# Kernel optimization log

Hardware: AMD Instinct MI355X
Metric: run time of the kernel (lower is better)

The kernel has to match this reference:

```python
import jax, jax.numpy as jnp
import numpy as np

N_NODES = 100000
EPS = 1e-12  # F.normalize eps


def _sage_conv(x, src, dst, deg, Wl, bl, Wr):
    # mean aggregation of neighbor (source) features at destination nodes
    agg = jax.ops.segment_sum(x[src], dst, num_segments=N_NODES)  # [N, F]
    agg = agg / jnp.maximum(deg, 1.0)[:, None]
    out = agg @ Wl + bl + x @ Wr  # lin_l(mean(x_j)) + lin_r(x_i)
    # normalize=True -> L2 row normalization
    norm = jnp.sqrt(jnp.sum(out * out, axis=-1, keepdims=True))
    return out / jnp.maximum(norm, EPS)


def setup_inputs() -> dict:
    key = jax.random.key(0)
    ks = jax.random.split(key, 10)
    F_IN, H, C = 14, 32, 2
    x = jax.random.normal(ks[0], (N_NODES, F_IN), dtype=jnp.float32)
    edge_index = jax.random.randint(ks[1], (2, 6400000), 0, N_NODES, dtype=jnp.int32)
    def glorot(k, shape):
        lim = float(np.sqrt(6.0 / (shape[0] + shape[1])))
        return jax.random.uniform(k, shape, jnp.float32, -lim, lim)
    return {
        "x": x,
        "edge_index": edge_index,
        "W1l": glorot(ks[2], (F_IN, H)), "b1": jnp.zeros((H,), jnp.float32),
        "W1r": glorot(ks[3], (F_IN, H)),
        "W2l": glorot(ks[4], (H, H)), "b2": jnp.zeros((H,), jnp.float32),
        "W2r": glorot(ks[5], (H, H)),
        "Wlin": glorot(ks[6], (H, C)), "blin": jnp.zeros((C,), jnp.float32),
    }


def reference(x, edge_index, W1l, b1, W1r, W2l, b2, W2r, Wlin, blin):
    src, dst = edge_index[0], edge_index[1]
    deg = jax.ops.segment_sum(jnp.ones_like(dst, dtype=x.dtype), dst,
                              num_segments=N_NODES)  # in-degree per node
    h = jax.nn.relu(_sage_conv(x, src, dst, deg, W1l, b1, W1r))
    # dropout p=0.2 is identity at inference
    h = jax.nn.relu(_sage_conv(h, src, dst, deg, W2l, b2, W2r))
    return h @ Wlin + blin  # [N, num_classes]
```

## Files before the change

### kernel.cpp

```cpp
#include <hip/hip_runtime.h>
#include <hip/hip_bf16.h>


#define CHA 16384
#define MAXB 512
#define CAPB 18432

static __device__ __forceinline__ unsigned short f2bf(float f) {
    unsigned u = __float_as_uint(f);
    unsigned r = (u + 0x7FFFu + ((u >> 16) & 1u)) >> 16;
    return (unsigned short)r;
}
#define BF_LO(u) __uint_as_float((u) << 16)
#define BF_HI(u) __uint_as_float((u) & 0xFFFF0000u)

__global__ void cvt_x_bf16(const float* __restrict__ x, unsigned short* __restrict__ xb,
                           int* __restrict__ bcursor, int N, int NB) {
    int idx = blockIdx.x * blockDim.x + threadIdx.x;
    if (idx < NB) bcursor[idx] = idx * CAPB;
    if (idx >= N * 16) return;
    int n = idx >> 4, f = idx & 15;
    float v = (f < 14) ? x[n * 14 + f] : 0.f;
    xb[idx] = f2bf(v);
}

__global__ __launch_bounds__(1024) void partitionA(
        const int* __restrict__ src, const int* __restrict__ dst,
        int* __restrict__ bcursor, unsigned* __restrict__ part, int E, int NB) {
    __shared__ unsigned pk[CHA];
    __shared__ int h[MAXB], lofs[MAXB], cur[MAXB], delta[MAXB], tmp[MAXB];
    int t = threadIdx.x;
    int base = blockIdx.x * CHA;
    int end = base + CHA; if (end > E) end = E;
    int cnt = end - base;

    int ed[16], es[16];
    for (int i = t; i < NB; i += 1024) h[i] = 0;
    __syncthreads();
    #pragma unroll
    for (int i = 0; i < 4; ++i) {
        int j = i * 4096 + t * 4;
        if (j + 4 <= cnt) {
            int4 d4 = *(const int4*)(dst + base + j);
            int4 s4 = *(const int4*)(src + base + j);
            ed[i*4+0] = d4.x; ed[i*4+1] = d4.y; ed[i*4+2] = d4.z; ed[i*4+3] = d4.w;
            es[i*4+0] = s4.x; es[i*4+1] = s4.y; es[i*4+2] = s4.z; es[i*4+3] = s4.w;
            atomicAdd(&h[d4.x >> 8], 1);
            atomicAdd(&h[d4.y >> 8], 1);
            atomicAdd(&h[d4.z >> 8], 1);
            atomicAdd(&h[d4.w >> 8], 1);
        } else {
            #pragma unroll
            for (int k = 0; k < 4; ++k) {
                if (j + k < cnt) {
                    ed[i*4+k] = dst[base + j + k];
                    es[i*4+k] = src[base + j + k];
                    atomicAdd(&h[ed[i*4+k] >> 8], 1);
                } else ed[i*4+k] = -1;
            }
        }
    }
    __syncthreads();
    int v = 0;
    if (t < MAXB) { v = (t < NB) ? h[t] : 0; tmp[t] = v; }
    __syncthreads();
    for (int off = 1; off < MAXB; off <<= 1) {
        int a = 0;
        if (t < MAXB && t >= off) a = tmp[t - off];
        __syncthreads();
        if (t < MAXB) tmp[t] += a;
        __syncthreads();
    }
    if (t < NB) {
        int excl = tmp[t] - v;
        lofs[t] = excl;
        cur[t] = excl;
        int g = v ? atomicAdd(&bcursor[t], v) : 0;
        delta[t] = g - excl;
    }
    __syncthreads();
    #pragma unroll
    for (int i = 0; i < 16; ++i) {
        int d = ed[i];
        if (d >= 0) {
            int b = d >> 8;
            int r = atomicAdd(&cur[b], 1);
            pk[r] = ((unsigned)(d & 255) << 24) | (unsigned)es[i];
        }
    }
    __syncthreads();
    int wid = t >> 6, lane = t & 63;
    for (int b = wid; b < NB; b += 16) {
        int s = lofs[b];
        int e2 = (b + 1 < NB) ? lofs[b + 1] : cnt;
        int dlt = delta[b];
        int lim = (b + 1) * CAPB;
        for (int k = s + lane; k < e2; k += 64) {
            int gidx = dlt + k;
            if (gidx < lim) part[gidx] = pk[k];
        }
    }
}

__global__ __launch_bounds__(1024) void partitionB_fused(
        const unsigned* __restrict__ part, const int* __restrict__ bcursor,
        const uint4* __restrict__ xb4, const float* __restrict__ x,
        const float* __restrict__ W1l, const float* __restrict__ b1,
        const float* __restrict__ W1r,
        int* __restrict__ deg, int* __restrict__ offs, int* __restrict__ nlo,
        int* __restrict__ sorted_src, float* __restrict__ hbuf,
        unsigned short* __restrict__ hb, int N, int HALF) {
    __shared__ int pk2[CAPB];
    __shared__ int hh[512], tmp[512], keyofs[512];
    __shared__ int lstart[256], ldeg[256];
    __shared__ float sagg[256 * 17];
    __shared__ float sx[256 * 14];
    __shared__ float swl[448], swr[448], sb1[32];
    int b = blockIdx.x;
    int t = threadIdx.x;
    int start = b * CAPB;
    int end = bcursor[b];
    if (end > start + CAPB) end = start + CAPB;
    int cnt = end - start;
    unsigned ce[18];
    if (t < 512) hh[t] = 0;
    if (t < 448) { swl[t] = W1l[t]; swr[t] = W1r[t]; }
    else if (t < 480) sb1[t - 448] = b1[t - 448];
    __syncthreads();
    #pragma unroll
    for (int i = 0; i < 18; ++i) {
        int idx = start + t + i * 1024;
        unsigned p = 0xFFFFFFFFu;
        if (idx < end) {
            p = part[idx];
            int key = (int)(p >> 24) * 2 + (((int)(p & 0xFFFFFFu) < HALF) ? 0 : 1);
            atomicAdd(&hh[key], 1);
        }
        ce[i] = p;
    }
    {
        int nnod = N - b * 256; if (nnod > 256) nnod = 256; if (nnod < 0) nnod = 0;
        const float* gx = x + (size_t)b * 256 * 14;
        for (int i = t; i < nnod * 14; i += 1024) sx[i] = gx[i];
    }
    __syncthreads();
    int v = (t < 512) ? hh[t] : 0;
    if (t < 512) tmp[t] = v;
    __syncthreads();
    for (int off = 1; off < 512; off <<= 1) {
        int a2 = (t < 512 && t >= off) ? tmp[t - off] : 0;
        __syncthreads();
        if (t < 512) tmp[t] += a2;
        __syncthreads();
    }
    if (t < 512) keyofs[t] = tmp[t] - v;
    __syncthreads();
    if (t < 256) {
        int lo = hh[2 * t];
        int d = lo + hh[2 * t + 1];
        int excl = keyofs[2 * t];
        lstart[t] = excl;
        ldeg[t] = d;
        int node = b * 256 + t;
        if (node < N) {
            deg[node] = d;
            offs[node] = start + excl;
            nlo[node] = lo;
        }
    }
    __syncthreads();
    #pragma unroll
    for (int i = 0; i < 18; ++i) {
        unsigned p = ce[i];
        if (p != 0xFFFFFFFFu) {
            int s = (int)(p & 0xFFFFFFu);
            int key = (int)(p >> 24) * 2 + ((s < HALF) ? 0 : 1);
            int r = atomicAdd(&keyofs[key], 1);
            pk2[r] = s;
        }
    }
    __syncthreads();
    for (int i = t; i < cnt; i += 1024)
        sorted_src[start + i] = pk2[i];

    int node = t >> 2, sub = t & 3, ep = sub >> 1, half = sub & 1;
    int js = lstart[node], d = ldeg[node];
    int je = js + d;
    float a[8] = {0,0,0,0,0,0,0,0};
    int j = js + ep;
    for (; j + 6 < je; j += 8) {
        int s0 = pk2[j], s1 = pk2[j+2], s2 = pk2[j+4], s3 = pk2[j+6];
        uint4 u0 = xb4[s0*2+half], u1 = xb4[s1*2+half], u2 = xb4[s2*2+half], u3 = xb4[s3*2+half];
        a[0] += BF_LO(u0.x)+BF_LO(u1.x)+BF_LO(u2.x)+BF_LO(u3.x);
        a[1] += BF_HI(u0.x)+BF_HI(u1.x)+BF_HI(u2.x)+BF_HI(u3.x);
        a[2] += BF_LO(u0.y)+BF_LO(u1.y)+BF_LO(u2.y)+BF_LO(u3.y);
        a[3] += BF_HI(u0.y)+BF_HI(u1.y)+BF_HI(u2.y)+BF_HI(u3.y);
        a[4] += BF_LO(u0.z)+BF_LO(u1.z)+BF_LO(u2.z)+BF_LO(u3.z);
        a[5] += BF_HI(u0.z)+BF_HI(u1.z)+BF_HI(u2.z)+BF_HI(u3.z);
        a[6] += BF_LO(u0.w)+BF_LO(u1.w)+BF_LO(u2.w)+BF_LO(u3.w);
        a[7] += BF_HI(u0.w)+BF_HI(u1.w)+BF_HI(u2.w)+BF_HI(u3.w);
    }
    for (; j < je; j += 2) {
        uint4 u0 = xb4[pk2[j]*2+half];
        a[0] += BF_LO(u0.x); a[1] += BF_HI(u0.x);
        a[2] += BF_LO(u0.y); a[3] += BF_HI(u0.y);
        a[4] += BF_LO(u0.z); a[5] += BF_HI(u0.z);
        a[6] += BF_LO(u0.w); a[7] += BF_HI(u0.w);
    }
    #pragma unroll
    for (int i = 0; i < 8; ++i) a[i] += __shfl_xor(a[i], 2);
    if (ep == 0) {
        #pragma unroll
        for (int i = 0; i < 8; ++i) sagg[node * 17 + half * 8 + i] = a[i];
    }
    __syncthreads();

    float inv = 1.0f / ((d > 0) ? (float)d : 1.0f);
    float acc[8];
    #pragma unroll
    for (int i = 0; i < 8; ++i) acc[i] = sb1[sub * 8 + i];
    #pragma unroll
    for (int k = 0; k < 14; ++k) {
        float ag = sagg[node * 17 + k] * inv;
        float xv = sx[node * 14 + k];
        const float4* wl4 = (const float4*)&swl[k * 32 + sub * 8];
        const float4* wr4 = (const float4*)&swr[k * 32 + sub * 8];
        float4 wla = wl4[0], wlb = wl4[1], wra = wr4[0], wrb = wr4[1];
        acc[0] += ag * wla.x + xv * wra.x;
        acc[1] += ag * wla.y + xv * wra.y;
        acc[2] += ag * wla.z + xv * wra.z;
        acc[3] += ag * wla.w + xv * wra.w;
        acc[4] += ag * wlb.x + xv * wrb.x;
        acc[5] += ag * wlb.y + xv * wrb.y;
        acc[6] += ag * wlb.z + xv * wrb.z;
        acc[7] += ag * wlb.w + xv * wrb.w;
    }
    float ss = 0.f;
    #pragma unroll
    for (int i = 0; i < 8; ++i) ss += acc[i] * acc[i];
    ss += __shfl_xor(ss, 1); ss += __shfl_xor(ss, 2);
    float invn = 1.f / fmaxf(sqrtf(ss), 1e-12f);
    int gnode = b * 256 + node;
    if (gnode < N) {
        float hv[8];
        #pragma unroll
        for (int i = 0; i < 8; ++i) hv[i] = fmaxf(acc[i] * invn, 0.f);
        float4* ho = (float4*)(hbuf + (size_t)gnode * 32 + sub * 8);
        ho[0] = make_float4(hv[0], hv[1], hv[2], hv[3]);
        ho[1] = make_float4(hv[4], hv[5], hv[6], hv[7]);
        uint4 pb;
        pb.x = (unsigned)f2bf(hv[0]) | ((unsigned)f2bf(hv[1]) << 16);
        pb.y = (unsigned)f2bf(hv[2]) | ((unsigned)f2bf(hv[3]) << 16);
        pb.z = (unsigned)f2bf(hv[4]) | ((unsigned)f2bf(hv[5]) << 16);
        pb.w = (unsigned)f2bf(hv[6]) | ((unsigned)f2bf(hv[7]) << 16);
        *(uint4*)(hb + (size_t)gnode * 32 + sub * 8) = pb;
    }
}

__global__ void gather32_p0(const uint4* __restrict__ hb, const int* __restrict__ sorted_src,
                            const int* __restrict__ offs, const int* __restrict__ nlo,
                            float4* __restrict__ agg2, int N) {
    int idx = blockIdx.x * blockDim.x + threadIdx.x;
    int n = idx >> 2;
    if (n >= N) return;
    int q = idx & 3;
    int start = offs[n];
    int jend = nlo[n];
    float a0=0,a1=0,a2=0,a3=0,a4=0,a5=0,a6=0,a7=0;
    int j = 0;
    for (; j + 4 <= jend; j += 4) {
        int s0 = sorted_src[start + j + 0];
        int s1 = sorted_src[start + j + 1];
        int s2 = sorted_src[start + j + 2];
        int s3 = sorted_src[start + j + 3];
        uint4 u0 = hb[s0 * 4 + q];
        uint4 u1 = hb[s1 * 4 + q];
        uint4 u2 = hb[s2 * 4 + q];
        uint4 u3 = hb[s3 * 4 + q];
        a0 += BF_LO(u0.x) + BF_LO(u1.x) + BF_LO(u2.x) + BF_LO(u3.x);
        a1 += BF_HI(u0.x) + BF_HI(u1.x) + BF_HI(u2.x) + BF_HI(u3.x);
        a2 += BF_LO(u0.y) + BF_LO(u1.y) + BF_LO(u2.y) + BF_LO(u3.y);
        a3 += BF_HI(u0.y) + BF_HI(u1.y) + BF_HI(u2.y) + BF_HI(u3.y);
        a4 += BF_LO(u0.z) + BF_LO(u1.z) + BF_LO(u2.z) + BF_LO(u3.z);
        a5 += BF_HI(u0.z) + BF_HI(u1.z) + BF_HI(u2.z) + BF_HI(u3.z);
        a6 += BF_LO(u0.w) + BF_LO(u1.w) + BF_LO(u2.w) + BF_LO(u3.w);
        a7 += BF_HI(u0.w) + BF_HI(u1.w) + BF_HI(u2.w) + BF_HI(u3.w);
    }
    for (; j < jend; ++j) {
        uint4 u0 = hb[sorted_src[start + j] * 4 + q];
        a0 += BF_LO(u0.x); a1 += BF_HI(u0.x);
        a2 += BF_LO(u0.y); a3 += BF_HI(u0.y);
        a4 += BF_LO(u0.z); a5 += BF_HI(u0.z);
        a6 += BF_LO(u0.w); a7 += BF_HI(u0.w);
    }
    agg2[n * 8 + q * 2 + 0] = make_float4(a0, a1, a2, a3);
    agg2[n * 8 + q * 2 + 1] = make_float4(a4, a5, a6, a7);
}

__global__ __launch_bounds__(256) void g32p1_dense2(
        const uint4* __restrict__ hb4, const int* __restrict__ sorted_src,
        const int* __restrict__ offs, const int* __restrict__ deg,
        const int* __restrict__ nlo, const float* __restrict__ agg2p,
        const float* __restrict__ hbuf,
        const float* __restrict__ W2l, const float* __restrict__ b2,
        const float* __restrict__ W2r, const float* __restrict__ Wlin,
        const float* __restrict__ blin, float* __restrict__ out, int N) {
    __shared__ float swl[1024], swr[1024], swo[64], sb2[32], sbo[2];
    int t = threadIdx.x;
    for (int i = t; i < 1024; i += 256) { swl[i] = W2l[i]; swr[i] = W2r[i]; }
    if (t < 64) swo[t] = Wlin[t];
    if (t < 32) sb2[t] = b2[t];
    if (t < 2) sbo[t] = blin[t];
    __syncthreads();
    int idx = blockIdx.x * 256 + t;
    int n = idx >> 2;
    if (n >= N) return;
    int q = idx & 3;
    int start = offs[n], d = deg[n], lo = nlo[n];
    float a[8] = {0,0,0,0,0,0,0,0};
    int j = lo;
    for (; j + 4 <= d; j += 4) {
        int s0 = sorted_src[start + j + 0];
        int s1 = sorted_src[start + j + 1];
        int s2 = sorted_src[start + j + 2];
        int s3 = sorted_src[start + j + 3];
        uint4 u0 = hb4[s0 * 4 + q];
        uint4 u1 = hb4[s1 * 4 + q];
        uint4 u2 = hb4[s2 * 4 + q];
        uint4 u3 = hb4[s3 * 4 + q];
        a[0] += BF_LO(u0.x)+BF_LO(u1.x)+BF_LO(u2.x)+BF_LO(u3.x);
        a[1] += BF_HI(u0.x)+BF_HI(u1.x)+BF_HI(u2.x)+BF_HI(u3.x);
        a[2] += BF_LO(u0.y)+BF_LO(u1.y)+BF_LO(u2.y)+BF_LO(u3.y);
        a[3] += BF_HI(u0.y)+BF_HI(u1.y)+BF_HI(u2.y)+BF_HI(u3.y);
        a[4] += BF_LO(u0.z)+BF_LO(u1.z)+BF_LO(u2.z)+BF_LO(u3.z);
        a[5] += BF_HI(u0.z)+BF_HI(u1.z)+BF_HI(u2.z)+BF_HI(u3.z);
        a[6] += BF_LO(u0.w)+BF_LO(u1.w)+BF_LO(u2.w)+BF_LO(u3.w);
        a[7] += BF_HI(u0.w)+BF_HI(u1.w)+BF_HI(u2.w)+BF_HI(u3.w);
    }
    for (; j < d; ++j) {
        uint4 u0 = hb4[sorted_src[start + j] * 4 + q];
        a[0] += BF_LO(u0.x); a[1] += BF_HI(u0.x);
        a[2] += BF_LO(u0.y); a[3] += BF_HI(u0.y);
        a[4] += BF_LO(u0.z); a[5] += BF_HI(u0.z);
        a[6] += BF_LO(u0.w); a[7] += BF_HI(u0.w);
    }
    float inv = 1.0f / ((d > 0) ? (float)d : 1.0f);
    const float4* gp = (const float4*)(agg2p + (size_t)n * 32 + q * 8);
    float4 p0 = gp[0], p1 = gp[1];
    float av[8];
    av[0] = (p0.x + a[0]) * inv; av[1] = (p0.y + a[1]) * inv;
    av[2] = (p0.z + a[2]) * inv; av[3] = (p0.w + a[3]) * inv;
    av[4] = (p1.x + a[4]) * inv; av[5] = (p1.y + a[5]) * inv;
    av[6] = (p1.z + a[6]) * inv; av[7] = (p1.w + a[7]) * inv;
    const float4* gh = (const float4*)(hbuf + (size_t)n * 32 + q * 8);
    float4 h0 = gh[0], h1 = gh[1];
    float hv8[8] = {h0.x, h0.y, h0.z, h0.w, h1.x, h1.y, h1.z, h1.w};
    float p[32];
    #pragma unroll
    for (int o = 0; o < 32; ++o) p[o] = 0.f;
    #pragma unroll
    for (int k = 0; k < 8; ++k) {
        int kk = q * 8 + k;
        const float4* wl4 = (const float4*)&swl[kk * 32];
        const float4* wr4 = (const float4*)&swr[kk * 32];
        #pragma unroll
        for (int o4 = 0; o4 < 8; ++o4) {
            float4 wl = wl4[o4], wr = wr4[o4];
            p[o4*4+0] += av[k] * wl.x + hv8[k] * wr.x;
            p[o4*4+1] += av[k] * wl.y + hv8[k] * wr.y;
            p[o4*4+2] += av[k] * wl.z + hv8[k] * wr.z;
            p[o4*4+3] += av[k] * wl.w + hv8[k] * wr.w;
        }
    }
    bool hi2 = (q & 2) != 0;
    float keep16[16];
    #pragma unroll
    for (int i = 0; i < 16; ++i) {
        float kv = hi2 ? p[i + 16] : p[i];
        float sv = hi2 ? p[i] : p[i + 16];
        keep16[i] = kv + __shfl_xor(sv, 2);
    }
    bool hi1 = (q & 1) != 0;
    float lin[8];
    #pragma unroll
    for (int i = 0; i < 8; ++i) {
        float kv = hi1 ? keep16[i + 8] : keep16[i];
        float sv = hi1 ? keep16[i] : keep16[i + 8];
        lin[i] = kv + __shfl_xor(sv, 1) + sb2[q * 8 + i];
    }
    float ss = 0.f;
    #pragma unroll
    for (int i = 0; i < 8; ++i) ss += lin[i] * lin[i];
    ss += __shfl_xor(ss, 1); ss += __shfl_xor(ss, 2);
    float invn = 1.f / fmaxf(sqrtf(ss), 1e-12f);
    float o0 = 0.f, o1 = 0.f;
    #pragma unroll
    for (int i = 0; i < 8; ++i) {
        float hv = fmaxf(lin[i] * invn, 0.f);
        int kk = q * 8 + i;
        o0 += hv * swo[kk * 2 + 0];
        o1 += hv * swo[kk * 2 + 1];
    }
    o0 += __shfl_xor(o0, 1); o0 += __shfl_xor(o0, 2);
    o1 += __shfl_xor(o1, 1); o1 += __shfl_xor(o1, 2);
    if (q == 0) {
        out[n * 2 + 0] = o0 + sbo[0];
        out[n * 2 + 1] = o1 + sbo[1];
    }
}

extern "C" void kernel_launch(void* const* d_in, const int* in_sizes, int n_in,
                              void* d_out, int out_size, void* d_ws, size_t ws_size,
                              hipStream_t stream) {
    const float* x    = (const float*)d_in[0];
    const int*   ei   = (const int*)d_in[1];
    const float* W1l  = (const float*)d_in[2];
    const float* b1   = (const float*)d_in[3];
    const float* W1r  = (const float*)d_in[4];
    const float* W2l  = (const float*)d_in[5];
    const float* b2   = (const float*)d_in[6];
    const float* W2r  = (const float*)d_in[7];
    const float* Wlin = (const float*)d_in[8];
    const float* blin = (const float*)d_in[9];
    float* out = (float*)d_out;

    const int N = in_sizes[0] / 14;
    const int E = in_sizes[1] / 2;
    const int* src = ei;
    const int* dst = ei + E;
    const int NB = (N + 255) / 256;
    const int HALF = N / 2;

    char* ws = (char*)d_ws;
    size_t off = 0;
    auto alloc = [&](size_t bytes) -> void* {
        void* p = ws + off;
        off = (off + bytes + 255) & ~(size_t)255;
        return p;
    };
    int*            bcursor    = (int*)alloc((size_t)NB * 4);
    unsigned*       part       = (unsigned*)alloc((size_t)NB * CAPB * 4);
    int*            sorted_src = (int*)alloc((size_t)NB * CAPB * 4);
    int*            deg        = (int*)alloc((size_t)N * 4);
    int*            offs       = (int*)alloc((size_t)N * 4);
    int*            nlo        = (int*)alloc((size_t)N * 4);
    unsigned short* xb         = (unsigned short*)alloc((size_t)N * 16 * 2);
    float*          hbuf       = (float*)alloc((size_t)N * 32 * 4);
    unsigned short* hb         = (unsigned short*)alloc((size_t)N * 32 * 2);
    float*          agg2       = (float*)part;
    (void)ws_size; (void)n_in; (void)out_size;

    cvt_x_bf16<<<(N * 16 + 255) / 256, 256, 0, stream>>>(x, xb, bcursor, N, NB);
    partitionA<<<(E + CHA - 1) / CHA, 1024, 0, stream>>>(src, dst, bcursor, part, E, NB);
    partitionB_fused<<<NB, 1024, 0, stream>>>(
        part, bcursor, (const uint4*)xb, x, W1l, b1, W1r,
        deg, offs, nlo, sorted_src, hbuf, hb, N, HALF);
    gather32_p0<<<(N * 4 + 255) / 256, 256, 0, stream>>>(
        (const uint4*)hb, sorted_src, offs, nlo, (float4*)agg2, N);
    g32p1_dense2<<<(N * 4 + 255) / 256, 256, 0, stream>>>(
        (const uint4*)hb, sorted_src, offs, deg, nlo, agg2, hbuf,
        W2l, b2, W2r, Wlin, blin, out, N);
}
```

Baseline: 298.6 us.

## Split fused layer-2 gather and dense into separate gather and smem-tiled dense kernels

Un-fuses the second-layer gather+dense kernel. One kernel now finishes the neighbor mean aggregation and writes it back to agg2. A new dense2 kernel stages 128 nodes of aggregate and self features in padded shared memory, then computes two nodes per thread with 8 outputs each. This lowers register pressure in the latency-bound gather kernel and cuts per-thread FMA work in the dense part. The cost is an extra launch and an extra global round trip of the aggregated features.

```diff
diff --git a/kernel.cpp b/kernel.cpp
--- a/kernel.cpp
+++ b/kernel.cpp
@@ -5,6 +5,7 @@
 #define CHA 16384
 #define MAXB 512
 #define CAPB 18432
+#define NPB 128
 
 static __device__ __forceinline__ unsigned short f2bf(float f) {
     unsigned u = __float_as_uint(f);
@@ -297,115 +298,124 @@
     agg2[n * 8 + q * 2 + 1] = make_float4(a4, a5, a6, a7);
 }
 
-__global__ __launch_bounds__(256) void g32p1_dense2(
-        const uint4* __restrict__ hb4, const int* __restrict__ sorted_src,
-        const int* __restrict__ offs, const int* __restrict__ deg,
-        const int* __restrict__ nlo, const float* __restrict__ agg2p,
-        const float* __restrict__ hbuf,
-        const float* __restrict__ W2l, const float* __restrict__ b2,
-        const float* __restrict__ W2r, const float* __restrict__ Wlin,
-        const float* __restrict__ blin, float* __restrict__ out, int N) {
-    __shared__ float swl[1024], swr[1024], swo[64], sb2[32], sbo[2];
-    int t = threadIdx.x;
-    for (int i = t; i < 1024; i += 256) { swl[i] = W2l[i]; swr[i] = W2r[i]; }
-    if (t < 64) swo[t] = Wlin[t];
-    if (t < 32) sb2[t] = b2[t];
-    if (t < 2) sbo[t] = blin[t];
-    __syncthreads();
-    int idx = blockIdx.x * 256 + t;
+__global__ void gather32_p1(const uint4* __restrict__ hb, const int* __restrict__ sorted_src,
+                            const int* __restrict__ offs, const int* __restrict__ deg,
+                            const int* __restrict__ nlo, float4* __restrict__ agg2, int N) {
+    int idx = blockIdx.x * blockDim.x + threadIdx.x;
     int n = idx >> 2;
     if (n >= N) return;
     int q = idx & 3;
-    int start = offs[n], d = deg[n], lo = nlo[n];
-    float a[8] = {0,0,0,0,0,0,0,0};
-    int j = lo;
+    int start = offs[n];
+    int d = deg[n];
+    int j = nlo[n];
+    float a0=0,a1=0,a2=0,a3=0,a4=0,a5=0,a6=0,a7=0;
     for (; j + 4 <= d; j += 4) {
         int s0 = sorted_src[start + j + 0];
         int s1 = sorted_src[start + j + 1];
         int s2 = sorted_src[start + j + 2];
         int s3 = sorted_src[start + j + 3];
-        uint4 u0 = hb4[s0 * 4 + q];
-        uint4 u1 = hb4[s1 * 4 + q];
-        uint4 u2 = hb4[s2 * 4 + q];
-        uint4 u3 = hb4[s3 * 4 + q];
-        a[0] += BF_LO(u0.x)+BF_LO(u1.x)+BF_LO(u2.x)+BF_LO(u3.x);
-        a[1] += BF_HI(u0.x)+BF_HI(u1.x)+BF_HI(u2.x)+BF_HI(u3.x);
-        a[2] += BF_LO(u0.y)+BF_LO(u1.y)+BF_LO(u2.y)+BF_LO(u3.y);
-        a[3] += BF_HI(u0.y)+BF_HI(u1.y)+BF_HI(u2.y)+BF_HI(u3.y);
-        a[4] += BF_LO(u0.z)+BF_LO(u1.z)+BF_LO(u2.z)+BF_LO(u3.z);
-        a[5] += BF_HI(u0.z)+BF_HI(u1.z)+BF_HI(u2.z)+BF_HI(u3.z);
-        a[6] += BF_LO(u0.w)+BF_LO(u1.w)+BF_LO(u2.w)+BF_LO(u3.w);
-        a[7] += BF_HI(u0.w)+BF_HI(u1.w)+BF_HI(u2.w)+BF_HI(u3.w);
+        uint4 u0 = hb[s0 * 4 + q];
+        uint4 u1 = hb[s1 * 4 + q];
+        uint4 u2 = hb[s2 * 4 + q];
+        uint4 u3 = hb[s3 * 4 + q];
+        a0 += BF_LO(u0.x) + BF_LO(u1.x) + BF_LO(u2.x) + BF_LO(u3.x);
+        a1 += BF_HI(u0.x) + BF_HI(u1.x) + BF_HI(u2.x) + BF_HI(u3.x);
+        a2 += BF_LO(u0.y) + BF_LO(u1.y) + BF_LO(u2.y) + BF_LO(u3.y);
+        a3 += BF_HI(u0.y) + BF_HI(u1.y) + BF_HI(u2.y) + BF_HI(u3.y);
+        a4 += BF_LO(u0.z) + BF_LO(u1.z) + BF_LO(u2.z) + BF_LO(u3.z);
+        a5 += BF_HI(u0.z) + BF_HI(u1.z) + BF_HI(u2.z) + BF_HI(u3.z);
+        a6 += BF_LO(u0.w) + BF_LO(u1.w) + BF_LO(u2.w) + BF_LO(u3.w);
+        a7 += BF_HI(u0.w) + BF_HI(u1.w) + BF_HI(u2.w) + BF_HI(u3.w);
     }
     for (; j < d; ++j) {
-        uint4 u0 = hb4[sorted_src[start + j] * 4 + q];
-        a[0] += BF_LO(u0.x); a[1] += BF_HI(u0.x);
-        a[2] += BF_LO(u0.y); a[3] += BF_HI(u0.y);
-        a[4] += BF_LO(u0.z); a[5] += BF_HI(u0.z);
-        a[6] += BF_LO(u0.w); a[7] += BF_HI(u0.w);
+        uint4 u0 = hb[sorted_src[start + j] * 4 + q];
+        a0 += BF_LO(u0.x); a1 += BF_HI(u0.x);
+        a2 += BF_LO(u0.y); a3 += BF_HI(u0.y);
+        a4 += BF_LO(u0.z); a5 += BF_HI(u0.z);
+        a6 += BF_LO(u0.w); a7 += BF_HI(u0.w);
     }
     float inv = 1.0f / ((d > 0) ? (float)d : 1.0f);
-    const float4* gp = (const float4*)(agg2p + (size_t)n * 32 + q * 8);
-    float4 p0 = gp[0], p1 = gp[1];
-    float av[8];
-    av[0] = (p0.x + a[0]) * inv; av[1] = (p0.y + a[1]) * inv;
-    av[2] = (p0.z + a[2]) * inv; av[3] = (p0.w + a[3]) * inv;
-    av[4] = (p1.x + a[4]) * inv; av[5] = (p1.y + a[5]) * inv;
-    av[6] = (p1.z + a[6]) * inv; av[7] = (p1.w + a[7]) * inv;
-    const float4* gh = (const float4*)(hbuf + (size_t)n * 32 + q * 8);
-    float4 h0 = gh[0], h1 = gh[1];
-    float hv8[8] = {h0.x, h0.y, h0.z, h0.w, h1.x, h1.y, h1.z, h1.w};
-    float p[32];
-    #pragma unroll
-    for (int o = 0; o < 32; ++o) p[o] = 0.f;
-    #pragma unroll
-    for (int k = 0; k < 8; ++k) {
-        int kk = q * 8 + k;
-        const float4* wl4 = (const float4*)&swl[kk * 32];
-        const float4* wr4 = (const float4*)&swr[kk * 32];
-        #pragma unroll
-        for (int o4 = 0; o4 < 8; ++o4) {
-            float4 wl = wl4[o4], wr = wr4[o4];
-            p[o4*4+0] += av[k] * wl.x + hv8[k] * wr.x;
-            p[o4*4+1] += av[k] * wl.y + hv8[k] * wr.y;
-            p[o4*4+2] += av[k] * wl.z + hv8[k] * wr.z;
-            p[o4*4+3] += av[k] * wl.w + hv8[k] * wr.w;
-        }
-    }
-    bool hi2 = (q & 2) != 0;
-    float keep16[16];
-    #pragma unroll
-    for (int i = 0; i < 16; ++i) {
-        float kv = hi2 ? p[i + 16] : p[i];
-        float sv = hi2 ? p[i] : p[i + 16];
-        keep16[i] = kv + __shfl_xor(sv, 2);
-    }
-    bool hi1 = (q & 1) != 0;
-    float lin[8];
-    #pragma unroll
-    for (int i = 0; i < 8; ++i) {
-        float kv = hi1 ? keep16[i + 8] : keep16[i];
-        float sv = hi1 ? keep16[i] : keep16[i + 8];
-        lin[i] = kv + __shfl_xor(sv, 1) + sb2[q * 8 + i];
-    }
-    float ss = 0.f;
-    #pragma unroll
-    for (int i = 0; i < 8; ++i) ss += lin[i] * lin[i];
-    ss += __shfl_xor(ss, 1); ss += __shfl_xor(ss, 2);
-    float invn = 1.f / fmaxf(sqrtf(ss), 1e-12f);
-    float o0 = 0.f, o1 = 0.f;
-    #pragma unroll
-    for (int i = 0; i < 8; ++i) {
-        float hv = fmaxf(lin[i] * invn, 0.f);
-        int kk = q * 8 + i;
-        o0 += hv * swo[kk * 2 + 0];
-        o1 += hv * swo[kk * 2 + 1];
-    }
-    o0 += __shfl_xor(o0, 1); o0 += __shfl_xor(o0, 2);
-    o1 += __shfl_xor(o1, 1); o1 += __shfl_xor(o1, 2);
-    if (q == 0) {
-        out[n * 2 + 0] = o0 + sbo[0];
-        out[n * 2 + 1] = o1 + sbo[1];
+    float4 p0 = agg2[n * 8 + q * 2 + 0];
+    float4 p1 = agg2[n * 8 + q * 2 + 1];
+    agg2[n * 8 + q * 2 + 0] = make_float4((p0.x + a0) * inv, (p0.y + a1) * inv,
+                                          (p0.z + a2) * inv, (p0.w + a3) * inv);
+    agg2[n * 8 + q * 2 + 1] = make_float4((p1.x + a4) * inv, (p1.y + a5) * inv,
+                                          (p1.z + a6) * inv, (p1.w + a7) * inv);
+}
+
+__global__ __launch_bounds__(256) void dense2(
+        const float* __restrict__ h, const float* __restrict__ agg2,
+        const float* __restrict__ W2l, const float* __restrict__ b2,
+        const float* __restrict__ W2r, const float* __restrict__ Wlin,
+        const float* __restrict__ blin, float* __restrict__ out, int N) {
+    __shared__ float sa[NPB * 33];
+    __shared__ float sh2[NPB * 33];
+    __shared__ float swl[32 * 32], swr[32 * 32], swo[64], sb[32], sbo[2];
+    int t = threadIdx.x;
+    int nb = blockIdx.x * NPB;
+    int nn = N - nb; if (nn > NPB) nn = NPB;
+    const float4* ga = (const float4*)(agg2 + (size_t)nb * 32);
+    const float4* gh = (const float4*)(h + (size_t)nb * 32);
+    for (int i = t; i < nn * 8; i += 256) {
+        float4 v = ga[i];
+        float* d = &sa[(i >> 3) * 33 + (i & 7) * 4];
+        d[0] = v.x; d[1] = v.y; d[2] = v.z; d[3] = v.w;
+        float4 w = gh[i];
+        float* e = &sh2[(i >> 3) * 33 + (i & 7) * 4];
+        e[0] = w.x; e[1] = w.y; e[2] = w.z; e[3] = w.w;
+    }
+    for (int i = t; i < 1024; i += 256) { swl[i] = W2l[i]; swr[i] = W2r[i]; }
+    if (t < 64) swo[t] = Wlin[t];
+    if (t < 32) sb[t] = b2[t];
+    if (t < 2) sbo[t] = blin[t];
+    __syncthreads();
+    int q2 = t & 3;
+    int p = t >> 2;
+    int l0 = p * 2, l1 = l0 + 1;
+    float acc0[8], acc1[8];
+    #pragma unroll
+    for (int j = 0; j < 8; ++j) { acc0[j] = sb[q2 * 8 + j]; acc1[j] = acc0[j]; }
+    for (int k = 0; k < 32; ++k) {
+        float a0 = sa[l0 * 33 + k],  a1 = sa[l1 * 33 + k];
+        float h0 = sh2[l0 * 33 + k], h1 = sh2[l1 * 33 + k];
+        const float4* wl4 = (const float4*)&swl[k * 32 + q2 * 8];
+        const float4* wr4 = (const float4*)&swr[k * 32 + q2 * 8];
+        float4 wla = wl4[0], wlb = wl4[1], wra = wr4[0], wrb = wr4[1];
+        acc0[0] += a0 * wla.x + h0 * wra.x;  acc1[0] += a1 * wla.x + h1 * wra.x;
+        acc0[1] += a0 * wla.y + h0 * wra.y;  acc1[1] += a1 * wla.y + h1 * wra.y;
+        acc0[2] += a0 * wla.z + h0 * wra.z;  acc1[2] += a1 * wla.z + h1 * wra.z;
+        acc0[3] += a0 * wla.w + h0 * wra.w;  acc1[3] += a1 * wla.w + h1 * wra.w;
+        acc0[4] += a0 * wlb.x + h0 * wrb.x;  acc1[4] += a1 * wlb.x + h1 * wrb.x;
+        acc0[5] += a0 * wlb.y + h0 * wrb.y;  acc1[5] += a1 * wlb.y + h1 * wrb.y;
+        acc0[6] += a0 * wlb.z + h0 * wrb.z;  acc1[6] += a1 * wlb.z + h1 * wrb.z;
+        acc0[7] += a0 * wlb.w + h0 * wrb.w;  acc1[7] += a1 * wlb.w + h1 * wrb.w;
+    }
+    float ss0 = 0.f, ss1 = 0.f;
+    #pragma unroll
+    for (int j = 0; j < 8; ++j) { ss0 += acc0[j] * acc0[j]; ss1 += acc1[j] * acc1[j]; }
+    ss0 += __shfl_xor(ss0, 1); ss0 += __shfl_xor(ss0, 2);
+    ss1 += __shfl_xor(ss1, 1); ss1 += __shfl_xor(ss1, 2);
+    float inv0 = 1.f / fmaxf(sqrtf(ss0), 1e-12f);
+    float inv1 = 1.f / fmaxf(sqrtf(ss1), 1e-12f);
+    float o00 = 0.f, o01 = 0.f, o10 = 0.f, o11 = 0.f;
+    #pragma unroll
+    for (int j = 0; j < 8; ++j) {
+        float hv0 = fmaxf(acc0[j] * inv0, 0.f);
+        float hv1 = fmaxf(acc1[j] * inv1, 0.f);
+        int kk = q2 * 8 + j;
+        o00 += hv0 * swo[kk * 2 + 0];
+        o01 += hv0 * swo[kk * 2 + 1];
+        o10 += hv1 * swo[kk * 2 + 0];
+        o11 += hv1 * swo[kk * 2 + 1];
+    }
+    o00 += __shfl_xor(o00, 1); o00 += __shfl_xor(o00, 2);
+    o01 += __shfl_xor(o01, 1); o01 += __shfl_xor(o01, 2);
+    o10 += __shfl_xor(o10, 1); o10 += __shfl_xor(o10, 2);
+    o11 += __shfl_xor(o11, 1); o11 += __shfl_xor(o11, 2);
+    if (q2 == 0) {
+        int n0 = nb + l0, n1 = nb + l1;
+        if (n0 < N) { out[n0 * 2 + 0] = o00 + sbo[0]; out[n0 * 2 + 1] = o01 + sbo[1]; }
+        if (n1 < N) { out[n1 * 2 + 0] = o10 + sbo[0]; out[n1 * 2 + 1] = o11 + sbo[1]; }
     }
 }
 
@@ -457,7 +467,8 @@
         deg, offs, nlo, sorted_src, hbuf, hb, N, HALF);
     gather32_p0<<<(N * 4 + 255) / 256, 256, 0, stream>>>(
         (const uint4*)hb, sorted_src, offs, nlo, (float4*)agg2, N);
-    g32p1_dense2<<<(N * 4 + 255) / 256, 256, 0, stream>>>(
-        (const uint4*)hb, sorted_src, offs, deg, nlo, agg2, hbuf,
-        W2l, b2, W2r, Wlin, blin, out, N);
-}
+    gather32_p1<<<(N * 4 + 255) / 256, 256, 0, stream>>>(
+        (const uint4*)hb, sorted_src, offs, deg, nlo, (float4*)agg2, N);
+    dense2<<<(N + NPB - 1) / NPB, 256, 0, stream>>>(
+        hbuf, agg2, W2l, b2, W2r, Wlin, blin, out, N);
+}
```

Result: faster. 273.2 us (-8.5%).
